# Optimization experiments

Hardware: AMD Instinct MI355X
Metric: run time of the kernel (lower is better)

The kernel has to match this reference:

```python
import jax, jax.numpy as jnp
import numpy as np
import math

N_HEADS = 4          # h2_dim*n_heads must equal g_dim for the stacked layers
H2_DIM = 32
G_DIM = 128
N_REL = 4
N_LAYERS = 2
PAST_W, FUT_W, PERIODIC = 5, 5, [15]
LN_EPS = 1e-5
BN_EPS = 1e-5


def _build_edges(d):
    ei, et = [], []
    for t in range(d):
        ei.append([t, t]); et.append(0)                      # self-loop
        for off in range(1, PAST_W + 1):
            if t - off >= 0:
                ei.append([t, t - off]); et.append(1)        # past
        for off in range(1, FUT_W + 1):
            if t + off < d:
                ei.append([t, t + off]); et.append(2)        # future
        for off in PERIODIC:
            if t + off < d:
                ei.append([t, t + off]); et.append(3)        # periodic fwd
            if t - off >= 0:
                ei.append([t, t - off]); et.append(3)        # periodic bwd
    return np.array(ei, dtype=np.int64).T, np.array(et, dtype=np.int64)


def setup_inputs() -> dict:
    key = jax.random.key(0)
    b, d, h, w, c = 4, 2048, 8, 8, 192
    ks = jax.random.split(key, 24)
    s = 0.05
    ei, et = _build_edges(d)
    inp = {
        'x': jax.random.normal(ks[0], (b, d, h, w, c), dtype=jnp.float32),
        'edge_index': jnp.asarray(ei),
        'edge_type': jnp.asarray(et),
        'fe_fc_w': jax.random.normal(ks[1], (c, G_DIM), dtype=jnp.float32) * s,
        'fe_fc_b': jnp.zeros((G_DIM,), jnp.float32),
        'fe_ln_g': jnp.ones((G_DIM,), jnp.float32),
        'fe_ln_b': jnp.zeros((G_DIM,), jnp.float32),
        'w_rel': jax.random.normal(ks[2], (N_LAYERS, N_REL, G_DIM, G_DIM), dtype=jnp.float32) * s,
        'w_root': jax.random.normal(ks[3], (N_LAYERS, G_DIM, G_DIM), dtype=jnp.float32) * s,
        'rgcn_b': jnp.zeros((N_LAYERS, G_DIM), jnp.float32),
        'wq': jax.random.normal(ks[4], (N_LAYERS, G_DIM, N_HEADS * H2_DIM), dtype=jnp.float32) * s,
        'bq': jnp.zeros((N_LAYERS, N_HEADS * H2_DIM), jnp.float32),
        'wk': jax.random.normal(ks[5], (N_LAYERS, G_DIM, N_HEADS * H2_DIM), dtype=jnp.float32) * s,
        'bk': jnp.zeros((N_LAYERS, N_HEADS * H2_DIM), jnp.float32),
        'wv': jax.random.normal(ks[6], (N_LAYERS, G_DIM, N_HEADS * H2_DIM), dtype=jnp.float32) * s,
        'bv': jnp.zeros((N_LAYERS, N_HEADS * H2_DIM), jnp.float32),
        'wskip': jax.random.normal(ks[7], (N_LAYERS, G_DIM, N_HEADS * H2_DIM), dtype=jnp.float32) * s,
        'bskip': jnp.zeros((N_LAYERS, N_HEADS * H2_DIM), jnp.float32),
        'bn_g': jnp.ones((N_LAYERS, N_HEADS * H2_DIM), jnp.float32),
        'bn_b': jnp.zeros((N_LAYERS, N_HEADS * H2_DIM), jnp.float32),
    }
    return inp


def _forward(x, edge_index, edge_type, fe_fc_w, fe_fc_b, fe_ln_g, fe_ln_b,
             w_rel, w_root, rgcn_b, wq, bq, wk, bk, wv, bv, wskip, bskip, bn_g, bn_b):
    d = x.shape[1]
    src, dst = edge_index[0], edge_index[1]
    rel_masks = [(edge_type == r).astype(jnp.float32) for r in range(N_REL)]
    inv_sqrt_c = 1.0 / math.sqrt(H2_DIM)

    def graph_fwd(xi):  # xi: [d,h,w,c]
        feat = xi.mean(axis=(1, 2))                         # adaptive avg pool -> [d,c]
        hfe = feat @ fe_fc_w + fe_fc_b                      # [d,g]
        mu = hfe.mean(-1, keepdims=True)
        var = ((hfe - mu) ** 2).mean(-1, keepdims=True)
        nf = (hfe - mu) / jnp.sqrt(var + LN_EPS) * fe_ln_g + fe_ln_b

        for l in range(N_LAYERS):
            # ---- RGCNConv (mean aggregation per relation + root) ----
            out = nf @ w_root[l] + rgcn_b[l]
            for r in range(N_REL):
                m = rel_masks[r]
                xr = nf @ w_rel[l, r]                       # [d,g]
                msg = xr[src] * m[:, None]                  # [E,g]
                s = jax.ops.segment_sum(msg, dst, num_segments=d)
                cnt = jax.ops.segment_sum(m, dst, num_segments=d)
                out = out + s / jnp.maximum(cnt, 1.0)[:, None]
            nf1 = out
            # ---- TransformerConv (per-head edge attention) ----
            q = (nf1 @ wq[l] + bq[l]).reshape(d, N_HEADS, H2_DIM)
            k = (nf1 @ wk[l] + bk[l]).reshape(d, N_HEADS, H2_DIM)
            v = (nf1 @ wv[l] + bv[l]).reshape(d, N_HEADS, H2_DIM)
            logits = (q[dst] * k[src]).sum(-1) * inv_sqrt_c  # [E,H]
            mx = jax.ops.segment_max(logits, dst, num_segments=d)
            a = jnp.exp(logits - mx[dst])
            denom = jax.ops.segment_sum(a, dst, num_segments=d)
            alpha = a / denom[dst]                           # softmax over incoming edges
            agg = jax.ops.segment_sum(alpha[:, :, None] * v[src], dst, num_segments=d)
            out2 = agg.reshape(d, N_HEADS * H2_DIM) + nf1 @ wskip[l] + bskip[l]
            # ---- BatchNorm1d (training-mode batch stats over nodes) ----
            bmu = out2.mean(0)
            bvar = ((out2 - bmu) ** 2).mean(0)
            out2 = (out2 - bmu) / jnp.sqrt(bvar + BN_EPS) * bn_g[l] + bn_b[l]
            nf = jax.nn.leaky_relu(out2, 0.01)
        return nf

    return jax.vmap(graph_fwd)(x)                           # [b,d,g]


def reference(x, edge_index, edge_type, fe_fc_w, fe_fc_b, fe_ln_g, fe_ln_b,
              w_rel, w_root, rgcn_b, wq, bq, wk, bk, wv, bv, wskip, bskip, bn_g, bn_b):
    return _forward(x, edge_index, edge_type, fe_fc_w, fe_fc_b, fe_ln_g, fe_ln_b,
                    w_rel, w_root, rgcn_b, wq, bq, wk, bk, wv, bv, wskip, bskip, bn_g, bn_b)
```

## Files before the change

### kernel.cpp

```cpp
#include <hip/hip_runtime.h>
#include <hip/hip_bf16.h>

#define B_ 4
#define D_ 2048
#define HWS 64
#define C_ 192
#define G_ 128
#define NODES (B_*D_)
#define R_ 16
#define HALO_ROWS 48

typedef short bf8_t  __attribute__((ext_vector_type(8)));
typedef float f32x4_t __attribute__((ext_vector_type(4)));

__device__ inline unsigned short f2bf(float f) {
    unsigned int u = __builtin_bit_cast(unsigned int, f);
    unsigned int r = (u + 0x7fffu + ((u >> 16) & 1u)) >> 16;
    return (unsigned short)r;
}
__device__ inline float bf2f(unsigned short h) {
    unsigned int u = ((unsigned int)h) << 16;
    return __builtin_bit_cast(float, u);
}

__device__ inline int xcd_swz(int x) { return (x & 7) * 64 + (x >> 3); }

struct WconvArgs {
    const float* src[16];
    const float* add[16];
};

__global__ __launch_bounds__(192) void pool_fc_ln_kernel(
    const float* __restrict__ x, const float* __restrict__ W,
    const float* __restrict__ bias, const float* __restrict__ gam,
    const float* __restrict__ bet, unsigned short* __restrict__ nf,
    WconvArgs wa, unsigned short* __restrict__ wbf)
{
    int u = blockIdx.x;
    int tid = threadIdx.x;
    __shared__ float feat[C_];
    __shared__ float4 red4[4][48];
    __shared__ float red[4];
    __shared__ float stats[2];

    const float4* xb4 = (const float4*)(x + (size_t)u * (HWS * C_));
    int cg = tid % 48;
    int rg = tid / 48;
    float4 a = make_float4(0.f, 0.f, 0.f, 0.f);
    #pragma unroll
    for (int s = 0; s < HWS; s += 4) {
        float4 v = xb4[(size_t)(s + rg) * 48 + cg];
        a.x += v.x; a.y += v.y; a.z += v.z; a.w += v.w;
    }
    red4[rg][cg] = a;
    __syncthreads();
    if (rg == 0) {
        float4 b0 = red4[0][cg], b1 = red4[1][cg], b2 = red4[2][cg], b3 = red4[3][cg];
        feat[cg * 4 + 0] = (b0.x + b1.x + b2.x + b3.x) * (1.0f / HWS);
        feat[cg * 4 + 1] = (b0.y + b1.y + b2.y + b3.y) * (1.0f / HWS);
        feat[cg * 4 + 2] = (b0.z + b1.z + b2.z + b3.z) * (1.0f / HWS);
        feat[cg * 4 + 3] = (b0.w + b1.w + b2.w + b3.w) * (1.0f / HWS);
    }
    __syncthreads();

    float h = 0.f;
    if (tid < G_) {
        h = bias[tid];
        #pragma unroll 4
        for (int c = 0; c < C_; ++c) h += feat[c] * W[c * G_ + tid];
    }
    float s1 = (tid < G_) ? h : 0.f;
    float s2 = (tid < G_) ? h * h : 0.f;
    #pragma unroll
    for (int off = 32; off >= 1; off >>= 1) {
        s1 += __shfl_xor(s1, off, 64);
        s2 += __shfl_xor(s2, off, 64);
    }
    int wid = tid >> 6;
    if ((tid & 63) == 0 && wid < 2) { red[wid] = s1; red[2 + wid] = s2; }
    __syncthreads();
    if (tid == 0) {
        float S = red[0] + red[1];
        float SS = red[2] + red[3];
        float mu = S / G_;
        float var = SS / G_ - mu * mu;
        stats[0] = mu;
        stats[1] = 1.0f / sqrtf(var + 1e-5f);
    }
    __syncthreads();
    if (tid < G_) {
        float v = (h - stats[0]) * stats[1] * gam[tid] + bet[tid];
        nf[(size_t)u * G_ + tid] = f2bf(v);
    }

    if (u < 2048 && tid < 128) {
        int idx = u * 128 + tid;
        int m = idx >> 14;
        int within = idx & 16383;
        int n = within >> 7, k = within & 127;
        float v = wa.src[m][k * G_ + n];
        if (wa.add[m]) v += wa.add[m][k * G_ + n];
        wbf[(size_t)m * 16384 + within] = f2bf(v);
    }
}

template <bool BNIN>
__global__ __launch_bounds__(256) void rgcn_fused_kernel(
    const unsigned short* __restrict__ nf, const float* __restrict__ xin,
    const float* __restrict__ partials, const float* __restrict__ gam,
    const float* __restrict__ bet,
    const unsigned short* __restrict__ wt,
    const float* __restrict__ rb,
    unsigned short* __restrict__ out)
{
    __shared__ char raw[HALO_ROWS * 256];
    __shared__ char agg[R_ * 1024];
    __shared__ float smu[G_], sivg[G_], sbet[G_];
    __shared__ float sred[2][G_], ssred[2][G_];
    int blk = xcd_swz(blockIdx.x);
    int b = blk >> 7;
    int t0 = (blk & 127) * R_;
    int tid = threadIdx.x;

    if constexpr (BNIN) {
        int halfk = tid >> 7;
        int c = tid & 127;
        float s = 0.f, ss = 0.f;
        const float* P = partials + (size_t)b * 128 * 256;
        #pragma unroll 4
        for (int k = halfk * 64; k < halfk * 64 + 64; ++k) {
            s += P[k * 256 + c];
            ss += P[k * 256 + G_ + c];
        }
        sred[halfk][c] = s;
        ssred[halfk][c] = ss;
        __syncthreads();
        if (tid < G_) {
            float S = sred[0][tid] + sred[1][tid];
            float SS = ssred[0][tid] + ssred[1][tid];
            float mu = S / D_;
            float var = SS / D_ - mu * mu;
            float inv = 1.0f / sqrtf(var + 1e-5f);
            smu[tid] = mu;
            sivg[tid] = inv * gam[tid];
            sbet[tid] = bet[tid];
        }
        __syncthreads();
        const float* xb = xin + (size_t)b * D_ * G_;
        #pragma unroll
        for (int p = 0; p < 3; ++p) {
            int task = tid + p * 256;
            int i = task >> 4, c16 = task & 15;
            int t = t0 - 15 + i;
            bf8_t v8 = {0, 0, 0, 0, 0, 0, 0, 0};
            if (t >= 0 && t < D_) {
                const float* vp = xb + (size_t)t * G_ + c16 * 8;
                #pragma unroll
                for (int e = 0; e < 8; ++e) {
                    int c = c16 * 8 + e;
                    float yv = (vp[e] - smu[c]) * sivg[c] + sbet[c];
                    yv = (yv > 0.f) ? yv : 0.01f * yv;
                    v8[e] = (short)f2bf(yv);
                }
            }
            *(bf8_t*)(raw + ((i * 256 + c16 * 16) ^ ((i & 7) << 4))) = v8;
        }
    } else {
        const unsigned short* src = nf + (size_t)b * D_ * G_;
        #pragma unroll
        for (int p = 0; p < 3; ++p) {
            int task = tid + p * 256;
            int i = task >> 4, c16 = task & 15;
            int t = t0 - 15 + i;
            bf8_t v = {0, 0, 0, 0, 0, 0, 0, 0};
            if (t >= 0 && t < D_) v = *(const bf8_t*)(src + (size_t)t * G_ + c16 * 8);
            *(bf8_t*)(raw + ((i * 256 + c16 * 16) ^ ((i & 7) << 4))) = v;
        }
    }
    __syncthreads();

    #pragma unroll
    for (int p = 0; p < 4; ++p) {
        int task = tid + p * 256;
        int c16 = task & 15, rel = (task >> 4) & 3, row = task >> 6;
        int t = t0 + row;
        int ctr = row + 15;
        float s[8] = {0.f,0.f,0.f,0.f,0.f,0.f,0.f,0.f};
        float scale = 1.f;
        if (rel == 0) {
            bf8_t v = *(const bf8_t*)(raw + ((ctr * 256 + c16 * 16) ^ ((ctr & 7) << 4)));
            #pragma unroll
            for (int e = 0; e < 8; ++e) s[e] = bf2f((unsigned short)v[e]);
        } else if (rel == 1) {
            #pragma unroll
            for (int o = 1; o <= 5; ++o) if (t + o < D_) {
                int i = ctr + o;
                bf8_t v = *(const bf8_t*)(raw + ((i * 256 + c16 * 16) ^ ((i & 7) << 4)));
                #pragma unroll
                for (int e = 0; e < 8; ++e) s[e] += bf2f((unsigned short)v[e]);
            }
            scale = 1.f / (float)max(min(5, D_ - 1 - t), 1);
        } else if (rel == 2) {
            #pragma unroll
            for (int o = 1; o <= 5; ++o) if (t - o >= 0) {
                int i = ctr - o;
                bf8_t v = *(const bf8_t*)(raw + ((i * 256 + c16 * 16) ^ ((i & 7) << 4)));
                #pragma unroll
                for (int e = 0; e < 8; ++e) s[e] += bf2f((unsigned short)v[e]);
            }
            scale = 1.f / (float)max(min(5, t), 1);
        } else {
            int cnt = 0;
            if (t >= 15) {
                int i = ctr - 15;
                bf8_t v = *(const bf8_t*)(raw + ((i * 256 + c16 * 16) ^ ((i & 7) << 4)));
                #pragma unroll
                for (int e = 0; e < 8; ++e) s[e] += bf2f((unsigned short)v[e]);
                cnt++;
            }
            if (t + 15 < D_) {
                int i = ctr + 15;
                bf8_t v = *(const bf8_t*)(raw + ((i * 256 + c16 * 16) ^ ((i & 7) << 4)));
                #pragma unroll
                for (int e = 0; e < 8; ++e) s[e] += bf2f((unsigned short)v[e]);
                cnt++;
            }
            scale = 1.f / (float)max(cnt, 1);
        }
        bf8_t o8;
        #pragma unroll
        for (int e = 0; e < 8; ++e) o8[e] = (short)f2bf(s[e] * scale);
        *(bf8_t*)(agg + ((row * 1024 + rel * 256 + c16 * 16) ^ ((row & 7) << 4))) = o8;
    }
    __syncthreads();

    int l = tid & 63, wv = tid >> 6;
    int l15 = l & 15, kgrp = l >> 4;
    int col16 = blockIdx.y * 4 + wv;
    f32x4_t acc = (f32x4_t){0.f, 0.f, 0.f, 0.f};

    for (int ks = 0; ks < 16; ++ks) {
        int rel = ks >> 2, kk = ks & 3;
        bf8_t a = *(const bf8_t*)(agg +
            ((l15 * 1024 + rel * 256 + kk * 64 + kgrp * 16) ^ ((l15 & 7) << 4)));
        bf8_t bf = *(const bf8_t*)(wt + rel * 16384 +
            (size_t)(col16 * 16 + l15) * G_ + kk * 32 + kgrp * 8);
        acc = __builtin_amdgcn_mfma_f32_16x16x32_bf16(a, bf, acc, 0, 0, 0);
    }

    unsigned short* outb = out + (size_t)b * D_ * G_;
    int rbase = t0 + kgrp * 4;
    int col = col16 * 16 + l15;
    float rbv = rb[col];
    #pragma unroll
    for (int j = 0; j < 4; ++j)
        outb[(size_t)(rbase + j) * G_ + col] = f2bf(acc[j] + rbv);
}

__device__ inline void stage_halo48(const unsigned short* __restrict__ src,
                                    int t0, char* raw, int tid)
{
    #pragma unroll
    for (int p = 0; p < 3; ++p) {
        int task = tid + p * 256;
        int i = task >> 4, c16 = task & 15;
        int t = t0 - 15 + i;
        bf8_t v = {0, 0, 0, 0, 0, 0, 0, 0};
        if (t >= 0 && t < D_) v = *(const bf8_t*)(src + (size_t)t * G_ + c16 * 8);
        *(bf8_t*)(raw + ((i * 256 + c16 * 16) ^ ((i & 7) << 4))) = v;
    }
}

__global__ __launch_bounds__(256) void qkvs_attn_kernel(
    const unsigned short* __restrict__ nf1,
    const unsigned short* __restrict__ wt,
    const float* __restrict__ bq, const float* __restrict__ bk,
    const float* __restrict__ bv, const float* __restrict__ bsk,
    float* __restrict__ out2, float* __restrict__ partials)
{
    __shared__ char raw[HALO_ROWS * 256];
    __shared__ unsigned short kls[HALO_ROWS * 64];
    __shared__ unsigned short vls[HALO_ROWS * 64];
    __shared__ unsigned short qls[R_ * 64];
    __shared__ float sls[R_ * 64];
    int blk = xcd_swz(blockIdx.x);
    int tid = threadIdx.x;
    int b = blk >> 7, t0 = (blk & 127) * R_;
    int y = blockIdx.y;

    stage_halo48(nf1 + (size_t)b * D_ * G_, t0, raw, tid);
    __syncthreads();

    int l = tid & 63, wvid = tid >> 6;
    int l15 = l & 15, kgrp = l >> 4;
    #pragma unroll
    for (int i = 0; i < 2; ++i) {
        int job = wvid + i * 4;
        int m, frag;
        if (job < 3)      { m = 1; frag = job; }
        else if (job < 6) { m = 2; frag = job - 3; }
        else if (job == 6){ m = 0; frag = 0; }
        else              { m = 3; frag = 0; }
        bool halo = (m == 1) | (m == 2);
        int rawrow = halo ? (frag * 16 + l15) : (15 + l15);
        const unsigned short* wm = wt + (size_t)m * 16384;
        const float* bias = (m == 0) ? bq : (m == 1) ? bk : (m == 2) ? bv : bsk;

        bf8_t a[4];
        #pragma unroll
        for (int kc = 0; kc < 4; ++kc)
            a[kc] = *(const bf8_t*)(raw +
                ((rawrow * 256 + kc * 64 + kgrp * 16) ^ ((rawrow & 7) << 4)));
        f32x4_t acc[4];
        #pragma unroll
        for (int n = 0; n < 4; ++n) acc[n] = (f32x4_t){0.f, 0.f, 0.f, 0.f};
        #pragma unroll
        for (int kc = 0; kc < 4; ++kc) {
            #pragma unroll
            for (int n = 0; n < 4; ++n) {
                int col = y * 64 + n * 16 + l15;
                bf8_t bf = *(const bf8_t*)(wm +
                    (size_t)col * G_ + kc * 32 + kgrp * 8);
                acc[n] = __builtin_amdgcn_mfma_f32_16x16x32_bf16(a[kc], bf, acc[n], 0, 0, 0);
            }
        }
        int r0 = frag * 16 + kgrp * 4;
        #pragma unroll
        for (int n = 0; n < 4; ++n) {
            int ln = n * 16 + l15;
            float bb = bias[y * 64 + ln];
            #pragma unroll
            for (int j = 0; j < 4; ++j) {
                float v = acc[n][j] + bb;
                int rr = r0 + j;
                if (m == 1)      kls[rr * 64 + ln] = f2bf(v);
                else if (m == 2) vls[rr * 64 + ln] = f2bf(v);
                else if (m == 0) qls[rr * 64 + ln] = f2bf(v);
                else             sls[rr * 64 + ln] = v;
            }
        }
    }
    __syncthreads();

    int j = tid & 63, quarter = tid >> 6;
    const float invs = 0.17677669529663687f;
    float ps = 0.f, pss = 0.f;
    float* o2b = out2 + (size_t)b * D_ * G_;
    const int offs[13] = {0, 1, 2, 3, 4, 5, -1, -2, -3, -4, -5, -15, 15};
    for (int it = 0; it < 4; ++it) {
        int tl = it * 4 + quarter;
        int t = t0 + tl;
        float q = bf2f(qls[tl * 64 + j]);
        float lg[13], vv[13];
        #pragma unroll
        for (int n = 0; n < 13; ++n) {
            int ts = t + offs[n];
            bool ok = (ts >= 0) && (ts < D_);
            int ki = tl + 15 + offs[n];
            float kk = ok ? bf2f(kls[ki * 64 + j]) : 0.f;
            vv[n] = ok ? bf2f(vls[ki * 64 + j]) : 0.f;
            float p = q * kk;
            p += __shfl_xor(p, 16, 32);
            p += __shfl_xor(p, 8, 32);
            p += __shfl_xor(p, 4, 32);
            p += __shfl_xor(p, 2, 32);
            p += __shfl_xor(p, 1, 32);
            lg[n] = ok ? p * invs : -1e30f;
        }
        float m = lg[0];
        #pragma unroll
        for (int n = 1; n < 13; ++n) m = fmaxf(m, lg[n]);
        float den = 0.f, aggv = 0.f;
        #pragma unroll
        for (int n = 0; n < 13; ++n) {
            float e = expf(lg[n] - m);
            den += e;
            aggv += e * vv[n];
        }
        float o = aggv / den + sls[tl * 64 + j];
        o2b[(size_t)t * G_ + y * 64 + j] = o;
        ps += o; pss += o * o;
    }

    __syncthreads();
    float* red = (float*)raw;
    red[quarter * 64 + j] = ps;
    red[256 + quarter * 64 + j] = pss;
    __syncthreads();
    if (tid < 64) {
        float s = 0.f, ss = 0.f;
        #pragma unroll
        for (int qq = 0; qq < 4; ++qq) {
            s += red[qq * 64 + tid];
            ss += red[256 + qq * 64 + tid];
        }
        float* P = partials + ((size_t)b * 128 + (blk & 127)) * 256;
        P[y * 64 + tid] = s;
        P[128 + y * 64 + tid] = ss;
    }
}

__global__ __launch_bounds__(256) void bn_apply_kernel(
    const float* __restrict__ X, const float* __restrict__ partials,
    const float* __restrict__ gam, const float* __restrict__ bet,
    float* __restrict__ out)
{
    int blk = blockIdx.x;
    int b = blk >> 7;
    int chunk = blk & 127;
    int tid = threadIdx.x;
    __shared__ float smu[G_], sinv[G_];
    __shared__ float sred[2][G_], ssred[2][G_];
    {
        int halfk = tid >> 7;
        int c = tid & 127;
        float s = 0.f, ss = 0.f;
        const float* P = partials + (size_t)b * 128 * 256;
        #pragma unroll 4
        for (int k = halfk * 64; k < halfk * 64 + 64; ++k) {
            s += P[k * 256 + c];
            ss += P[k * 256 + G_ + c];
        }
        sred[halfk][c] = s;
        ssred[halfk][c] = ss;
    }
    __syncthreads();
    if (tid < G_) {
        float S = sred[0][tid] + sred[1][tid];
        float SS = ssred[0][tid] + ssred[1][tid];
        float mu = S / D_;
        float var = SS / D_ - mu * mu;
        smu[tid] = mu;
        sinv[tid] = 1.0f / sqrtf(var + 1e-5f);
    }
    __syncthreads();

    const float4* base4 = (const float4*)(X + ((size_t)b * D_ + chunk * 16) * G_);
    float4* ob4 = (float4*)(out + ((size_t)b * D_ + chunk * 16) * G_);
    int c4 = (tid & 31) * 4;
    float m0 = smu[c4], m1 = smu[c4 + 1], m2 = smu[c4 + 2], m3 = smu[c4 + 3];
    float i0 = sinv[c4] * gam[c4],     i1 = sinv[c4 + 1] * gam[c4 + 1];
    float i2 = sinv[c4 + 2] * gam[c4 + 2], i3 = sinv[c4 + 3] * gam[c4 + 3];
    float b0 = bet[c4], b1 = bet[c4 + 1], b2 = bet[c4 + 2], b3 = bet[c4 + 3];
    #pragma unroll
    for (int p = 0; p < 2; ++p) {
        float4 v = base4[p * 256 + tid];
        float4 y;
        y.x = (v.x - m0) * i0 + b0;
        y.y = (v.y - m1) * i1 + b1;
        y.z = (v.z - m2) * i2 + b2;
        y.w = (v.w - m3) * i3 + b3;
        y.x = (y.x > 0.f) ? y.x : 0.01f * y.x;
        y.y = (y.y > 0.f) ? y.y : 0.01f * y.y;
        y.z = (y.z > 0.f) ? y.z : 0.01f * y.z;
        y.w = (y.w > 0.f) ? y.w : 0.01f * y.w;
        ob4[p * 256 + tid] = y;
    }
}

extern "C" void kernel_launch(void* const* d_in, const int* in_sizes, int n_in,
                              void* d_out, int out_size, void* d_ws, size_t ws_size,
                              hipStream_t stream)
{
    (void)in_sizes; (void)n_in; (void)out_size; (void)ws_size;
    const float* x      = (const float*)d_in[0];
    const float* fe_w   = (const float*)d_in[3];
    const float* fe_b   = (const float*)d_in[4];
    const float* ln_g   = (const float*)d_in[5];
    const float* ln_b   = (const float*)d_in[6];
    const float* w_rel  = (const float*)d_in[7];
    const float* w_root = (const float*)d_in[8];
    const float* rgcn_b = (const float*)d_in[9];
    const float* wq  = (const float*)d_in[10];
    const float* bq  = (const float*)d_in[11];
    const float* wk  = (const float*)d_in[12];
    const float* bk  = (const float*)d_in[13];
    const float* wv  = (const float*)d_in[14];
    const float* bv  = (const float*)d_in[15];
    const float* wsk = (const float*)d_in[16];
    const float* bsk = (const float*)d_in[17];
    const float* bn_g = (const float*)d_in[18];
    const float* bn_b = (const float*)d_in[19];

    float* ws   = (float*)d_ws;
    float* out2 = ws;
    float* partials = out2 + (size_t)NODES * G_;
    unsigned short* nf_bf  = (unsigned short*)(partials + 4 * 128 * 256);
    unsigned short* nf1_bf = nf_bf + (size_t)NODES * G_;
    unsigned short* wbf    = nf1_bf + (size_t)NODES * G_;

    WconvArgs wa;
    for (int l = 0; l < 2; ++l) {
        for (int r = 0; r < 4; ++r) {
            wa.src[l * 8 + r] = w_rel + ((size_t)l * 4 + r) * G_ * G_;
            wa.add[l * 8 + r] = (r == 0) ? (w_root + (size_t)l * G_ * G_) : nullptr;
        }
        wa.src[l * 8 + 4] = wq  + (size_t)l * G_ * G_; wa.add[l * 8 + 4] = nullptr;
        wa.src[l * 8 + 5] = wk  + (size_t)l * G_ * G_; wa.add[l * 8 + 5] = nullptr;
        wa.src[l * 8 + 6] = wv  + (size_t)l * G_ * G_; wa.add[l * 8 + 6] = nullptr;
        wa.src[l * 8 + 7] = wsk + (size_t)l * G_ * G_; wa.add[l * 8 + 7] = nullptr;
    }

    pool_fc_ln_kernel<<<NODES, 192, 0, stream>>>(
        x, fe_w, fe_b, ln_g, ln_b, nf_bf, wa, wbf);

    rgcn_fused_kernel<false><<<dim3(512, 2), 256, 0, stream>>>(
        nf_bf, nullptr, nullptr, nullptr, nullptr,
        wbf, rgcn_b, nf1_bf);
    qkvs_attn_kernel<<<dim3(512, 2), 256, 0, stream>>>(
        nf1_bf, wbf + (size_t)4 * 16384,
        bq, bk, bv, bsk, out2, partials);

    rgcn_fused_kernel<true><<<dim3(512, 2), 256, 0, stream>>>(
        nullptr, out2, partials, bn_g, bn_b,
        wbf + (size_t)8 * 16384, rgcn_b + G_, nf1_bf);
    qkvs_attn_kernel<<<dim3(512, 2), 256, 0, stream>>>(
        nf1_bf, wbf + (size_t)12 * 16384,
        bq + G_, bk + G_, bv + G_, bsk + G_, out2, partials);

    bn_apply_kernel<<<512, 256, 0, stream>>>(
        out2, partials, bn_g + G_, bn_b + G_, (float*)d_out);
}
```

Before: 209.2 us.

## Merge column-split blocks into single 512-thread blocks for rgcn and attention kernels

The two column-half blocks per 16-row tile (grid y=2) are merged into one 512-thread block that covers all 128 output columns. The halo staging, relation aggregation and BN-stat reduction now run once per tile instead of twice, which removes the duplicated global loads and aggregation work. In exchange the block count halves to 512 and LDS per block for K/V/Q/skip doubles, which may reduce occupancy and latency hiding.

Measured after the change: 207.6 us. Within noise of the previous version (-0.7%).

```diff
diff --git a/kernel.cpp b/kernel.cpp
--- a/kernel.cpp
+++ b/kernel.cpp
@@ -105,7 +105,7 @@
 }
 
 template <bool BNIN>
-__global__ __launch_bounds__(256) void rgcn_fused_kernel(
+__global__ __launch_bounds__(512, 4) void rgcn_fused_kernel(
     const unsigned short* __restrict__ nf, const float* __restrict__ xin,
     const float* __restrict__ partials, const float* __restrict__ gam,
     const float* __restrict__ bet,
@@ -123,17 +123,19 @@
     int tid = threadIdx.x;
 
     if constexpr (BNIN) {
-        int halfk = tid >> 7;
-        int c = tid & 127;
-        float s = 0.f, ss = 0.f;
-        const float* P = partials + (size_t)b * 128 * 256;
-        #pragma unroll 4
-        for (int k = halfk * 64; k < halfk * 64 + 64; ++k) {
-            s += P[k * 256 + c];
-            ss += P[k * 256 + G_ + c];
-        }
-        sred[halfk][c] = s;
-        ssred[halfk][c] = ss;
+        if (tid < 256) {
+            int halfk = tid >> 7;
+            int c = tid & 127;
+            float s = 0.f, ss = 0.f;
+            const float* P = partials + (size_t)b * 128 * 256;
+            #pragma unroll 4
+            for (int k = halfk * 64; k < halfk * 64 + 64; ++k) {
+                s += P[k * 256 + c];
+                ss += P[k * 256 + G_ + c];
+            }
+            sred[halfk][c] = s;
+            ssred[halfk][c] = ss;
+        }
         __syncthreads();
         if (tid < G_) {
             float S = sred[0][tid] + sred[1][tid];
@@ -148,40 +150,44 @@
         __syncthreads();
         const float* xb = xin + (size_t)b * D_ * G_;
         #pragma unroll
-        for (int p = 0; p < 3; ++p) {
-            int task = tid + p * 256;
-            int i = task >> 4, c16 = task & 15;
-            int t = t0 - 15 + i;
-            bf8_t v8 = {0, 0, 0, 0, 0, 0, 0, 0};
-            if (t >= 0 && t < D_) {
-                const float* vp = xb + (size_t)t * G_ + c16 * 8;
-                #pragma unroll
-                for (int e = 0; e < 8; ++e) {
-                    int c = c16 * 8 + e;
-                    float yv = (vp[e] - smu[c]) * sivg[c] + sbet[c];
-                    yv = (yv > 0.f) ? yv : 0.01f * yv;
-                    v8[e] = (short)f2bf(yv);
+        for (int p = 0; p < 2; ++p) {
+            int task = tid + p * 512;
+            if (task < HALO_ROWS * 16) {
+                int i = task >> 4, c16 = task & 15;
+                int t = t0 - 15 + i;
+                bf8_t v8 = {0, 0, 0, 0, 0, 0, 0, 0};
+                if (t >= 0 && t < D_) {
+                    const float* vp = xb + (size_t)t * G_ + c16 * 8;
+                    #pragma unroll
+                    for (int e = 0; e < 8; ++e) {
+                        int c = c16 * 8 + e;
+                        float yv = (vp[e] - smu[c]) * sivg[c] + sbet[c];
+                        yv = (yv > 0.f) ? yv : 0.01f * yv;
+                        v8[e] = (short)f2bf(yv);
+                    }
                 }
-            }
-            *(bf8_t*)(raw + ((i * 256 + c16 * 16) ^ ((i & 7) << 4))) = v8;
+                *(bf8_t*)(raw + ((i * 256 + c16 * 16) ^ ((i & 7) << 4))) = v8;
+            }
         }
     } else {
         const unsigned short* src = nf + (size_t)b * D_ * G_;
         #pragma unroll
-        for (int p = 0; p < 3; ++p) {
-            int task = tid + p * 256;
-            int i = task >> 4, c16 = task & 15;
-            int t = t0 - 15 + i;
-            bf8_t v = {0, 0, 0, 0, 0, 0, 0, 0};
-            if (t >= 0 && t < D_) v = *(const bf8_t*)(src + (size_t)t * G_ + c16 * 8);
-            *(bf8_t*)(raw + ((i * 256 + c16 * 16) ^ ((i & 7) << 4))) = v;
+        for (int p = 0; p < 2; ++p) {
+            int task = tid + p * 512;
+            if (task < HALO_ROWS * 16) {
+                int i = task >> 4, c16 = task & 15;
+                int t = t0 - 15 + i;
+                bf8_t v = {0, 0, 0, 0, 0, 0, 0, 0};
+                if (t >= 0 && t < D_) v = *(const bf8_t*)(src + (size_t)t * G_ + c16 * 8);
+                *(bf8_t*)(raw + ((i * 256 + c16 * 16) ^ ((i & 7) << 4))) = v;
+            }
         }
     }
     __syncthreads();
 
     #pragma unroll
-    for (int p = 0; p < 4; ++p) {
-        int task = tid + p * 256;
+    for (int p = 0; p < 2; ++p) {
+        int task = tid + p * 512;
         int c16 = task & 15, rel = (task >> 4) & 3, row = task >> 6;
         int t = t0 + row;
         int ctr = row + 15;
@@ -236,7 +242,7 @@
 
     int l = tid & 63, wv = tid >> 6;
     int l15 = l & 15, kgrp = l >> 4;
-    int col16 = blockIdx.y * 4 + wv;
+    int col16 = wv;
     f32x4_t acc = (f32x4_t){0.f, 0.f, 0.f, 0.f};
 
     for (int ks = 0; ks < 16; ++ks) {
@@ -257,21 +263,7 @@
         outb[(size_t)(rbase + j) * G_ + col] = f2bf(acc[j] + rbv);
 }
 
-__device__ inline void stage_halo48(const unsigned short* __restrict__ src,
-                                    int t0, char* raw, int tid)
-{
-    #pragma unroll
-    for (int p = 0; p < 3; ++p) {
-        int task = tid + p * 256;
-        int i = task >> 4, c16 = task & 15;
-        int t = t0 - 15 + i;
-        bf8_t v = {0, 0, 0, 0, 0, 0, 0, 0};
-        if (t >= 0 && t < D_) v = *(const bf8_t*)(src + (size_t)t * G_ + c16 * 8);
-        *(bf8_t*)(raw + ((i * 256 + c16 * 16) ^ ((i & 7) << 4))) = v;
-    }
-}
-
-__global__ __launch_bounds__(256) void qkvs_attn_kernel(
+__global__ __launch_bounds__(512, 4) void qkvs_attn_kernel(
     const unsigned short* __restrict__ nf1,
     const unsigned short* __restrict__ wt,
     const float* __restrict__ bq, const float* __restrict__ bk,
@@ -279,28 +271,41 @@
     float* __restrict__ out2, float* __restrict__ partials)
 {
     __shared__ char raw[HALO_ROWS * 256];
-    __shared__ unsigned short kls[HALO_ROWS * 64];
-    __shared__ unsigned short vls[HALO_ROWS * 64];
-    __shared__ unsigned short qls[R_ * 64];
-    __shared__ float sls[R_ * 64];
+    __shared__ unsigned short kls[HALO_ROWS * 128];
+    __shared__ unsigned short vls[HALO_ROWS * 128];
+    __shared__ unsigned short qls[R_ * 128];
+    __shared__ float sls[R_ * 128];
     int blk = xcd_swz(blockIdx.x);
     int tid = threadIdx.x;
     int b = blk >> 7, t0 = (blk & 127) * R_;
-    int y = blockIdx.y;
-
-    stage_halo48(nf1 + (size_t)b * D_ * G_, t0, raw, tid);
+
+    {
+        const unsigned short* src = nf1 + (size_t)b * D_ * G_;
+        #pragma unroll
+        for (int p = 0; p < 2; ++p) {
+            int task = tid + p * 512;
+            if (task < HALO_ROWS * 16) {
+                int i = task >> 4, c16 = task & 15;
+                int t = t0 - 15 + i;
+                bf8_t v = {0, 0, 0, 0, 0, 0, 0, 0};
+                if (t >= 0 && t < D_) v = *(const bf8_t*)(src + (size_t)t * G_ + c16 * 8);
+                *(bf8_t*)(raw + ((i * 256 + c16 * 16) ^ ((i & 7) << 4))) = v;
+            }
+        }
+    }
     __syncthreads();
 
     int l = tid & 63, wvid = tid >> 6;
     int l15 = l & 15, kgrp = l >> 4;
     #pragma unroll
     for (int i = 0; i < 2; ++i) {
-        int job = wvid + i * 4;
+        int job = wvid + i * 8;
+        int y = job >> 3, jj = job & 7;
         int m, frag;
-        if (job < 3)      { m = 1; frag = job; }
-        else if (job < 6) { m = 2; frag = job - 3; }
-        else if (job == 6){ m = 0; frag = 0; }
-        else              { m = 3; frag = 0; }
+        if (jj < 3)      { m = 1; frag = jj; }
+        else if (jj < 6) { m = 2; frag = jj - 3; }
+        else if (jj == 6){ m = 0; frag = 0; }
+        else             { m = 3; frag = 0; }
         bool halo = (m == 1) | (m == 2);
         int rawrow = halo ? (frag * 16 + l15) : (15 + l15);
         const unsigned short* wm = wt + (size_t)m * 16384;
@@ -327,38 +332,38 @@
         int r0 = frag * 16 + kgrp * 4;
         #pragma unroll
         for (int n = 0; n < 4; ++n) {
-            int ln = n * 16 + l15;
-            float bb = bias[y * 64 + ln];
+            int gc = y * 64 + n * 16 + l15;
+            float bb = bias[gc];
             #pragma unroll
             for (int j = 0; j < 4; ++j) {
                 float v = acc[n][j] + bb;
                 int rr = r0 + j;
-                if (m == 1)      kls[rr * 64 + ln] = f2bf(v);
-                else if (m == 2) vls[rr * 64 + ln] = f2bf(v);
-                else if (m == 0) qls[rr * 64 + ln] = f2bf(v);
-                else             sls[rr * 64 + ln] = v;
-            }
-        }
-    }
-    __syncthreads();
-
-    int j = tid & 63, quarter = tid >> 6;
+                if (m == 1)      kls[rr * 128 + gc] = f2bf(v);
+                else if (m == 2) vls[rr * 128 + gc] = f2bf(v);
+                else if (m == 0) qls[rr * 128 + gc] = f2bf(v);
+                else             sls[rr * 128 + gc] = v;
+            }
+        }
+    }
+    __syncthreads();
+
+    int j = tid & 127, grp = tid >> 7;
     const float invs = 0.17677669529663687f;
     float ps = 0.f, pss = 0.f;
     float* o2b = out2 + (size_t)b * D_ * G_;
     const int offs[13] = {0, 1, 2, 3, 4, 5, -1, -2, -3, -4, -5, -15, 15};
     for (int it = 0; it < 4; ++it) {
-        int tl = it * 4 + quarter;
+        int tl = it * 4 + grp;
         int t = t0 + tl;
-        float q = bf2f(qls[tl * 64 + j]);
+        float q = bf2f(qls[tl * 128 + j]);
         float lg[13], vv[13];
         #pragma unroll
         for (int n = 0; n < 13; ++n) {
             int ts = t + offs[n];
             bool ok = (ts >= 0) && (ts < D_);
             int ki = tl + 15 + offs[n];
-            float kk = ok ? bf2f(kls[ki * 64 + j]) : 0.f;
-            vv[n] = ok ? bf2f(vls[ki * 64 + j]) : 0.f;
+            float kk = ok ? bf2f(kls[ki * 128 + j]) : 0.f;
+            vv[n] = ok ? bf2f(vls[ki * 128 + j]) : 0.f;
             float p = q * kk;
             p += __shfl_xor(p, 16, 32);
             p += __shfl_xor(p, 8, 32);
@@ -377,26 +382,26 @@
             den += e;
             aggv += e * vv[n];
         }
-        float o = aggv / den + sls[tl * 64 + j];
-        o2b[(size_t)t * G_ + y * 64 + j] = o;
+        float o = aggv / den + sls[tl * 128 + j];
+        o2b[(size_t)t * G_ + j] = o;
         ps += o; pss += o * o;
     }
 
     __syncthreads();
     float* red = (float*)raw;
-    red[quarter * 64 + j] = ps;
-    red[256 + quarter * 64 + j] = pss;
-    __syncthreads();
-    if (tid < 64) {
+    red[grp * 128 + j] = ps;
+    red[512 + grp * 128 + j] = pss;
+    __syncthreads();
+    if (tid < 128) {
         float s = 0.f, ss = 0.f;
         #pragma unroll
-        for (int qq = 0; qq < 4; ++qq) {
-            s += red[qq * 64 + tid];
-            ss += red[256 + qq * 64 + tid];
+        for (int g = 0; g < 4; ++g) {
+            s += red[g * 128 + tid];
+            ss += red[512 + g * 128 + tid];
         }
         float* P = partials + ((size_t)b * 128 + (blk & 127)) * 256;
-        P[y * 64 + tid] = s;
-        P[128 + y * 64 + tid] = ss;
+        P[tid] = s;
+        P[128 + tid] = ss;
     }
 }
 
@@ -504,17 +509,17 @@
     pool_fc_ln_kernel<<<NODES, 192, 0, stream>>>(
         x, fe_w, fe_b, ln_g, ln_b, nf_bf, wa, wbf);
 
-    rgcn_fused_kernel<false><<<dim3(512, 2), 256, 0, stream>>>(
+    rgcn_fused_kernel<false><<<512, 512, 0, stream>>>(
         nf_bf, nullptr, nullptr, nullptr, nullptr,
         wbf, rgcn_b, nf1_bf);
-    qkvs_attn_kernel<<<dim3(512, 2), 256, 0, stream>>>(
+    qkvs_attn_kernel<<<512, 512, 0, stream>>>(
         nf1_bf, wbf + (size_t)4 * 16384,
         bq, bk, bv, bsk, out2, partials);
 
-    rgcn_fused_kernel<true><<<dim3(512, 2), 256, 0, stream>>>(
+    rgcn_fused_kernel<true><<<512, 512, 0, stream>>>(
         nullptr, out2, partials, bn_g, bn_b,
         wbf + (size_t)8 * 16384, rgcn_b + G_, nf1_bf);
-    qkvs_attn_kernel<<<dim3(512, 2), 256, 0, stream>>>(
+    qkvs_attn_kernel<<<512, 512, 0, stream>>>(
         nf1_bf, wbf + (size_t)12 * 16384,
         bq + G_, bk + G_, bv + G_, bsk + G_, out2, partials);
 
```
